# Optimization experiments

Hardware: AMD Instinct MI355X
Metric: run time of the kernel (lower is better)

The kernel has to match this reference:

```python
import jax, jax.numpy as jnp
import numpy as np

M = 5
N = 3
NUM_EPOC = 500
LR = 0.01


def setup_inputs() -> dict:
    key = jax.random.key(0)
    k1, k2, k3, k4, k5 = jax.random.split(key, 5)
    x = jax.random.normal(k1, (8, 32, 32, 128), dtype=jnp.float32)
    weight = jax.random.normal(k2, (3, 3, 128, 256), dtype=jnp.float32) * 0.05
    shiftPara = jax.random.normal(k3, (N,), dtype=jnp.float32) * 0.1
    beta = jax.random.normal(k4, (N,), dtype=jnp.float32)
    alphas_init = jax.random.normal(k5, (M,), dtype=jnp.float32)
    return {"x": x, "weight": weight, "shiftPara": shiftPara, "beta": beta, "alphas_init": alphas_init}


def _binary_weights(w):
    # w: (kh, kw, Cin, Cout). sign(W - mean + shift_i * std), shift_i in linspace(-1, 1, M)
    mean = jnp.mean(w)
    var = jnp.var(w)
    shifts = (-1.0 + jnp.arange(M, dtype=jnp.float32) * (2.0 / (M - 1))) * jnp.sqrt(var)  # (M,)
    return jnp.sign((w - mean)[None] + shifts.reshape(M, 1, 1, 1, 1))  # (M, kh, kw, Cin, Cout)


def _alphas(w, bw, alphas_init):
    # 500-step OLS gradient descent, faithful to the original loop
    flat_w = w.reshape(-1)            # (K,)
    flat_b = bw.reshape(M, -1)        # (M, K)
    K = flat_w.shape[0]

    def step(a, _):
        resid = flat_b.T @ a - flat_w            # (K,)
        grad = (flat_b @ resid) / K              # (M,)
        return a - LR * grad, None

    a, _ = jax.lax.scan(step, alphas_init, None, length=NUM_EPOC)
    return a


def reference(x, weight, shiftPara, beta, alphas_init):
    B, H, W, Cin = x.shape
    kh, kw, _, Cout = weight.shape

    bw = _binary_weights(weight)                       # (M, kh, kw, Cin, Cout)
    alphas = _alphas(weight, bw, alphas_init)          # (M,)

    # N binarized input branches: sign(clip(x + shift_n, 0, 1) - 0.5)
    shifted = jnp.clip(x[None] + shiftPara.reshape(N, 1, 1, 1, 1), 0.0, 1.0)
    bx = jnp.sign(shifted - 0.5)                       # (N, B, H, W, Cin)

    # Fold the M binary bases into output channels -> single conv over N*B images
    w_all = jnp.transpose(bw, (1, 2, 3, 0, 4)).reshape(kh, kw, Cin, M * Cout)
    y = jax.lax.conv_general_dilated(
        bx.reshape(N * B, H, W, Cin), w_all,
        window_strides=(1, 1), padding="SAME",
        dimension_numbers=("NHWC", "HWIO", "NHWC"))     # (N*B, H, W, M*Cout)
    y = y.reshape(N, B, H, W, M, Cout)

    # sum_m alpha_m * conv, then sum_n beta_n * branch
    return jnp.einsum("nbhwmc,m,n->bhwc", y, alphas, beta)
```

## Files before the change

### kernel.cpp

```cpp
#include <hip/hip_runtime.h>
#include <math.h>

#define KW_ELEMS 294912
#define KW_F4    73728
#define LR_GD 0.01
#define NBLK_RED 64
#define NBLK_XE  192
#define NBLK_GC  256

typedef __attribute__((ext_vector_type(8))) short short8;
typedef __attribute__((ext_vector_type(4))) float f32x4;

#define WS_SP_OFF    0
#define WS_GP_OFF    1024
#define WS_WP_OFF    17408
#define WS_XE_OFF    607232
#define XE_CHUNKS    (8 * 34 * 34 * 16)

__device__ __forceinline__ unsigned short f2bf(float f) {
    union { float f; unsigned int u; } v; v.f = f;
    unsigned int r = v.u + 0x7fffu + ((v.u >> 16) & 1u);
    return (unsigned short)(r >> 16);
}

__device__ __forceinline__ void read_stats(const double* sp, double& sw, double& sw2) {
    int lane = threadIdx.x & 63;
    double a = sp[2 * lane];
    double b = sp[2 * lane + 1];
    #pragma unroll
    for (int off = 32; off > 0; off >>= 1) {
        a += __shfl_xor(a, off, 64);
        b += __shfl_xor(b, off, 64);
    }
    sw = a; sw2 = b;
}

__device__ __forceinline__ float xeff_one(float xv, float s0, float s1, float s2,
                                          float be0, float be1, float be2) {
    float v0 = xv + s0, v1 = xv + s1, v2 = xv + s2;
    float g0 = (v0 > 0.5f) ? 1.0f : ((v0 < 0.5f) ? -1.0f : 0.0f);
    float g1 = (v1 > 0.5f) ? 1.0f : ((v1 < 0.5f) ? -1.0f : 0.0f);
    float g2 = (v2 > 0.5f) ? 1.0f : ((v2 < 0.5f) ? -1.0f : 0.0f);
    return be0 * g0 + be1 * g1 + be2 * g2;
}

__global__ __launch_bounds__(256) void k_pre(const float* __restrict__ w,
                                             const float* __restrict__ x,
                                             const float* __restrict__ shiftp,
                                             const float* __restrict__ beta,
                                             void* __restrict__ wsv) {
    int tid = threadIdx.x;

    if (blockIdx.x < NBLK_RED) {
        double* sp = (double*)((char*)wsv + WS_SP_OFF);
        __shared__ double s1[256];
        __shared__ double s2[256];

        double a = 0.0, b = 0.0;
        for (int i4 = blockIdx.x * 256 + tid; i4 < KW_F4; i4 += NBLK_RED * 256) {
            float4 v = *(const float4*)(&w[i4 * 4]);
            a += (double)v.x + (double)v.y + (double)v.z + (double)v.w;
            b += (double)v.x * (double)v.x + (double)v.y * (double)v.y
               + (double)v.z * (double)v.z + (double)v.w * (double)v.w;
        }
        s1[tid] = a; s2[tid] = b;
        __syncthreads();
        for (int off = 128; off > 0; off >>= 1) {
            if (tid < off) { s1[tid] += s1[tid + off]; s2[tid] += s2[tid + off]; }
            __syncthreads();
        }
        if (tid == 0) { sp[blockIdx.x * 2] = s1[0]; sp[blockIdx.x * 2 + 1] = s2[0]; }
    } else {
        unsigned short* xe = (unsigned short*)((char*)wsv + WS_XE_OFF);
        float s0 = shiftp[0], s1v = shiftp[1], s2v = shiftp[2];
        float be0 = beta[0], be1 = beta[1], be2 = beta[2];

        for (int idx = (blockIdx.x - NBLK_RED) * 256 + tid; idx < XE_CHUNKS;
             idx += NBLK_XE * 256) {
            int cb  = idx & 15;
            int c2  = idx >> 4;
            int pos = c2 % 34;
            int t   = c2 / 34;
            int row = t % 34;
            int b   = t / 34;
            int g   = row - 1;
            int wp  = pos - 1;
            unsigned short v[8] = {0, 0, 0, 0, 0, 0, 0, 0};
            if (g >= 0 && g < 32 && wp >= 0 && wp < 32) {
                const float* xp = &x[(((b * 32 + g) * 32) + wp) * 128 + cb * 8];
                float4 x0 = *(const float4*)(xp);
                float4 x1 = *(const float4*)(xp + 4);
                float e[8] = {x0.x, x0.y, x0.z, x0.w, x1.x, x1.y, x1.z, x1.w};
                #pragma unroll
                for (int j = 0; j < 8; j++)
                    v[j] = f2bf(xeff_one(e[j], s0, s1v, s2v, be0, be1, be2));
            }
            int dst = c2 * 256 + ((cb * 16) ^ ((pos & 7) << 4));
            *(short8*)((char*)xe + dst) = *(short8*)v;
        }
    }
}

__global__ __launch_bounds__(256) void k_gc(const float* __restrict__ w,
                                            void* __restrict__ wsv) {
    const double* sp = (const double*)((const char*)wsv + WS_SP_OFF);
    char* gp = (char*)wsv + WS_GP_OFF;

    __shared__ int    lg[4][5];
    __shared__ double lc[4][5];

    int tid  = threadIdx.x;
    int lane = tid & 63;
    int wave = tid >> 6;

    double sw, sw2;
    read_stats(sp, sw, sw2);
    double mean = sw / (double)KW_ELEMS;
    double var  = sw2 / (double)KW_ELEMS - mean * mean;
    float meanf = (float)mean;
    float sigf  = sqrtf((float)var);

    float thr[5];
    #pragma unroll
    for (int m = 0; m < 5; m++) thr[m] = (1.0f - 0.5f * (float)m) * sigf;

    int   cnt[5] = {0, 0, 0, 0, 0};
    float ss[5]  = {0.f, 0.f, 0.f, 0.f, 0.f};
    for (int i4 = blockIdx.x * 256 + tid; i4 < KW_F4; i4 += NBLK_GC * 256) {
        float4 v = *(const float4*)(&w[i4 * 4]);
        float e[4] = {v.x, v.y, v.z, v.w};
        #pragma unroll
        for (int j = 0; j < 4; j++) {
            float base = e[j] - meanf;
            #pragma unroll
            for (int m = 0; m < 5; m++) {
                bool bel = base < thr[m];
                cnt[m] += bel ? 1 : 0;
                ss[m]  += bel ? e[j] : 0.f;
            }
        }
    }
    double sd[5];
    #pragma unroll
    for (int m = 0; m < 5; m++) sd[m] = (double)ss[m];
    #pragma unroll
    for (int m = 0; m < 5; m++) {
        int c = cnt[m]; double s = sd[m];
        #pragma unroll
        for (int off = 32; off > 0; off >>= 1) {
            c += __shfl_xor(c, off, 64);
            s += __shfl_xor(s, off, 64);
        }
        cnt[m] = c; sd[m] = s;
    }
    if (lane == 0) {
        #pragma unroll
        for (int m = 0; m < 5; m++) { lg[wave][m] = cnt[m]; lc[wave][m] = sd[m]; }
    }
    __syncthreads();
    if (tid == 0) {
        int*    pn = (int*)(gp + blockIdx.x * 64);
        double* pS = (double*)(gp + blockIdx.x * 64 + 24);
        #pragma unroll
        for (int m = 0; m < 5; m++) {
            pn[m] = lg[0][m] + lg[1][m] + lg[2][m] + lg[3][m];
            pS[m] = lc[0][m] + lc[1][m] + lc[2][m] + lc[3][m];
        }
    }
}

__global__ __launch_bounds__(256) void k_weff(const float* __restrict__ w,
                                              const float* __restrict__ a0f,
                                              void* __restrict__ wsv) {
    const double* sp = (const double*)((const char*)wsv + WS_SP_OFF);
    const char*   gp = (const char*)wsv + WS_GP_OFF;
    unsigned short* wpk = (unsigned short*)((char*)wsv + WS_WP_OFF);

    __shared__ double Gd[25];
    __shared__ double RmL[25];
    __shared__ double astar_s[5];
    __shared__ float  alph[5];
    __shared__ float  tile[32][64];

    int tid   = threadIdx.x;
    int lane  = tid & 63;
    int tap   = blockIdx.x >> 4;
    int rest  = blockIdx.x & 15;
    int c32   = rest >> 2;
    int cin0  = c32 * 32;
    int cout0 = (rest & 3) * 64;

    int i0 = tid, i1 = tid + 256;
    int ci0 = i0 >> 4, f40 = i0 & 15;
    int ci1 = i1 >> 4, f41 = i1 & 15;
    float4 v0 = *(const float4*)(&w[(tap * 128 + cin0 + ci0) * 256 + cout0 + f40 * 4]);
    float4 v1 = *(const float4*)(&w[(tap * 128 + cin0 + ci1) * 256 + cout0 + f41 * 4]);

    double sw, sw2;
    read_stats(sp, sw, sw2);
    double mean = sw / (double)KW_ELEMS;
    double var  = sw2 / (double)KW_ELEMS - mean * mean;
    float meanf = (float)mean;
    float sigf  = sqrtf((float)var);

    int nred[5]; double Sred[5];
    #pragma unroll
    for (int m = 0; m < 5; m++) { nred[m] = 0; Sred[m] = 0.0; }
    #pragma unroll
    for (int q = 0; q < 4; q++) {
        const int*    pn = (const int*)(gp + (lane + q * 64) * 64);
        const double* pS = (const double*)(gp + (lane + q * 64) * 64 + 24);
        #pragma unroll
        for (int m = 0; m < 5; m++) { nred[m] += pn[m]; Sred[m] += pS[m]; }
    }
    #pragma unroll
    for (int m = 0; m < 5; m++) {
        int c = nred[m]; double s = Sred[m];
        #pragma unroll
        for (int off = 32; off > 0; off >>= 1) {
            c += __shfl_xor(c, off, 64);
            s += __shfl_xor(s, off, 64);
        }
        nred[m] = c; Sred[m] = s;
    }
    double Creg[5];
    #pragma unroll
    for (int m = 0; m < 5; m++)
        Creg[m] = (sw - 2.0 * Sred[m]) / (double)KW_ELEMS;

    double Rg = 0.0, Ag = 0.0;
    {
        int i = tid / 5, j = tid % 5;
        if (tid < 25) {
            double v;
            if (i == j) v = 1.0;
            else {
                int d = nred[i] - nred[j];
                if (d < 0) d = -d;
                v = ((double)KW_ELEMS - 2.0 * (double)d) / (double)KW_ELEMS;
            }
            Gd[tid] = v;
            Ag = ((i == j) ? 1.0 : 0.0) - LR_GD * v;
            Rg = Ag;
        }
    }
    __syncthreads();

    if (tid == 64) {
        double L[25];
        #pragma unroll
        for (int i = 0; i < 25; i++) L[i] = 0.0;
        #pragma unroll
        for (int i = 0; i < 5; i++) {
            #pragma unroll
            for (int j = 0; j <= i; j++) {
                double s = Gd[i * 5 + j];
                #pragma unroll
                for (int k = 0; k < j; k++) s -= L[i * 5 + k] * L[j * 5 + k];
                if (i == j) L[i * 5 + j] = sqrt(s);
                else        L[i * 5 + j] = s / L[j * 5 + j];
            }
        }
        double y[5], astar[5];
        #pragma unroll
        for (int i = 0; i < 5; i++) {
            double s = Creg[i];
            #pragma unroll
            for (int k = 0; k < i; k++) s -= L[i * 5 + k] * y[k];
            y[i] = s / L[i * 5 + i];
        }
        #pragma unroll
        for (int ii2 = 0; ii2 < 5; ii2++) {
            int i = 4 - ii2;
            double s = y[i];
            #pragma unroll
            for (int k = 0; k < 5; k++) if (k > i) s -= L[k * 5 + i] * astar[k];
            astar[i] = s / L[i * 5 + i];
        }
        #pragma unroll
        for (int i = 0; i < 5; i++) astar_s[i] = astar[i];
    }

    if (tid < 25) {
        int i = tid / 5, j = tid % 5;
        const int bits[8] = {1, 1, 1, 1, 0, 1, 0, 0};
        #pragma unroll
        for (int s = 0; s < 8; s++) {
            double t = 0.0;
            #pragma unroll
            for (int k = 0; k < 5; k++) {
                double rik = __shfl(Rg, i * 5 + k, 64);
                double rkj = __shfl(Rg, k * 5 + j, 64);
                t += rik * rkj;
            }
            if (bits[s]) {
                double r2 = 0.0;
                #pragma unroll
                for (int k = 0; k < 5; k++) {
                    double tik = __shfl(t, i * 5 + k, 64);
                    double akj = __shfl(Ag, k * 5 + j, 64);
                    r2 += tik * akj;
                }
                Rg = r2;
            } else {
                Rg = t;
            }
        }
        RmL[tid] = Rg;
    }
    __syncthreads();

    if (tid < 5) {
        double s = astar_s[tid];
        #pragma unroll
        for (int j = 0; j < 5; j++)
            s += RmL[tid * 5 + j] * ((double)a0f[j] - astar_s[j]);
        alph[tid] = (float)s;
    }
    __syncthreads();

    float al[5] = {alph[0], alph[1], alph[2], alph[3], alph[4]};

    {
        float r[4] = {v0.x, v0.y, v0.z, v0.w};
        #pragma unroll
        for (int j = 0; j < 4; j++) {
            float base = r[j] - meanf;
            float acc = 0.0f;
            #pragma unroll
            for (int m = 0; m < 5; m++) {
                float arg = base + (-1.0f + 0.5f * (float)m) * sigf;
                float s = (arg > 0.0f) ? 1.0f : ((arg < 0.0f) ? -1.0f : 0.0f);
                acc += al[m] * s;
            }
            tile[ci0][f40 * 4 + j] = acc;
        }
        float r1[4] = {v1.x, v1.y, v1.z, v1.w};
        #pragma unroll
        for (int j = 0; j < 4; j++) {
            float base = r1[j] - meanf;
            float acc = 0.0f;
            #pragma unroll
            for (int m = 0; m < 5; m++) {
                float arg = base + (-1.0f + 0.5f * (float)m) * sigf;
                float s = (arg > 0.0f) ? 1.0f : ((arg < 0.0f) ? -1.0f : 0.0f);
                acc += al[m] * s;
            }
            tile[ci1][f41 * 4 + j] = acc;
        }
    }
    __syncthreads();

    int cc  = tid & 63;
    int kg  = tid >> 6;
    unsigned short ob[8];
    #pragma unroll
    for (int k = 0; k < 8; k++) ob[k] = f2bf(tile[kg * 8 + k][cc]);
    unsigned short* dst = wpk + (((tap * 16 + c32 * 4 + kg) * 256) + cout0 + cc) * 8;
    *(short8*)dst = *(short8*)ob;
}

__global__ __launch_bounds__(256, 2) void k_conv(
    const void* __restrict__ wsv, float* __restrict__ out) {
    const unsigned short* wp = (const unsigned short*)((const char*)wsv + WS_WP_OFF);
    const char* xe = (const char*)wsv + WS_XE_OFF;
    __shared__ __align__(16) unsigned short ldsx[3 * 34 * 128];

    int bid = blockIdx.x;
    int ch  = bid & 1;
    int h   = (bid >> 1) & 31;
    int b   = bid >> 6;
    int tid = threadIdx.x;

    const char* src = xe + ((b * 34 + h) * 34) * 256;
    #pragma unroll 2
    for (int i = tid; i < 1632; i += 256) {
        *(short8*)((char*)ldsx + i * 16) = *(const short8*)(src + i * 16);
    }
    __syncthreads();

    int lane = tid & 63;
    int wave = tid >> 6;
    int l15  = lane & 15;
    int kg   = lane >> 4;
    int coutbase = (ch << 7) + wave * 32;

    f32x4 acc[2][2];
    #pragma unroll
    for (int mt = 0; mt < 2; mt++)
        #pragma unroll
        for (int nt = 0; nt < 2; nt++) acc[mt][nt] = (f32x4){0.f, 0.f, 0.f, 0.f};

    const unsigned short* wbase = wp + ((kg * 256) + coutbase + l15) * 8;

    short8 bc[8], bn[8];
    #pragma unroll
    for (int q = 0; q < 4; q++) {
        bc[2 * q]     = *(const short8*)(wbase + q * 8192);
        bc[2 * q + 1] = *(const short8*)(wbase + q * 8192 + 128);
    }

    #pragma unroll
    for (int dh = 0; dh < 3; dh++) {
        #pragma unroll
        for (int dw = 0; dw < 3; dw++) {
            int tap = dh * 3 + dw;
            if (tap < 8) {
                const unsigned short* wnx = wbase + (tap + 1) * 32768;
                #pragma unroll
                for (int q = 0; q < 4; q++) {
                    bn[2 * q]     = *(const short8*)(wnx + q * 8192);
                    bn[2 * q + 1] = *(const short8*)(wnx + q * 8192 + 128);
                }
            }
            int r0  = dh * 34 + l15 + dw;
            int r1  = r0 + 16;
            int key = ((l15 + dw) & 7) << 4;
            #pragma unroll
            for (int q = 0; q < 4; q++) {
                int cbyte = q * 64 + kg * 16;
                short8 a0f8 = *(const short8*)((const char*)ldsx +
                               (r0 * 256 + (cbyte ^ key)));
                short8 a1f8 = *(const short8*)((const char*)ldsx +
                               (r1 * 256 + (cbyte ^ key)));
                acc[0][0] = __builtin_amdgcn_mfma_f32_16x16x32_bf16(a0f8, bc[2*q],   acc[0][0], 0, 0, 0);
                acc[0][1] = __builtin_amdgcn_mfma_f32_16x16x32_bf16(a0f8, bc[2*q+1], acc[0][1], 0, 0, 0);
                acc[1][0] = __builtin_amdgcn_mfma_f32_16x16x32_bf16(a1f8, bc[2*q],   acc[1][0], 0, 0, 0);
                acc[1][1] = __builtin_amdgcn_mfma_f32_16x16x32_bf16(a1f8, bc[2*q+1], acc[1][1], 0, 0, 0);
            }
            if (tap < 8) {
                #pragma unroll
                for (int i = 0; i < 8; i++) bc[i] = bn[i];
            }
        }
    }

    #pragma unroll
    for (int mt = 0; mt < 2; mt++) {
        #pragma unroll
        for (int nt = 0; nt < 2; nt++) {
            int col = coutbase + nt * 16 + l15;
            #pragma unroll
            for (int reg = 0; reg < 4; reg++) {
                int row = mt * 16 + kg * 4 + reg;
                out[(((b * 32 + h) * 32) + row) * 256 + col] = acc[mt][nt][reg];
            }
        }
    }
}

extern "C" void kernel_launch(void* const* d_in, const int* in_sizes, int n_in,
                              void* d_out, int out_size, void* d_ws, size_t ws_size,
                              hipStream_t stream) {
    const float* x      = (const float*)d_in[0];
    const float* w      = (const float*)d_in[1];
    const float* shiftp = (const float*)d_in[2];
    const float* beta   = (const float*)d_in[3];
    const float* a0     = (const float*)d_in[4];
    float* out = (float*)d_out;

    k_pre<<<NBLK_RED + NBLK_XE, 256, 0, stream>>>(w, x, shiftp, beta, d_ws);
    k_gc<<<NBLK_GC, 256, 0, stream>>>(w, d_ws);
    k_weff<<<144, 256, 0, stream>>>(w, a0, d_ws);
    k_conv<<<512, 256, 0, stream>>>(d_ws, out);
}
```

Measured before the change: 30.49 us.

## Split input binarization across k_gc and k_weff to fill idle blocks

The input-encoding work (xe) moves out of the first preprocessing kernel and is split into two halves. Each half runs on extra blocks appended to k_gc and to k_weff, so it overlaps the latency-bound weight-statistics and alpha/weight-packing stages. k_pre now only does the weight sum reduction with 64 blocks. The intent is to shorten the critical path by using idle CUs in the small kernels. The risk is that the extra blocks compete with the stages they share a kernel with and lengthen them.

New measurement: 31.36 us. 1.03x slower.

```diff
diff --git a/kernel.cpp b/kernel.cpp
--- a/kernel.cpp
+++ b/kernel.cpp
@@ -5,8 +5,8 @@
 #define KW_F4    73728
 #define LR_GD 0.01
 #define NBLK_RED 64
-#define NBLK_XE  192
 #define NBLK_GC  256
+#define NBLK_XR  128
 
 typedef __attribute__((ext_vector_type(8))) short short8;
 typedef __attribute__((ext_vector_type(4))) float f32x4;
@@ -16,6 +16,7 @@
 #define WS_WP_OFF    17408
 #define WS_XE_OFF    607232
 #define XE_CHUNKS    (8 * 34 * 34 * 16)
+#define XE_HALF      (XE_CHUNKS / 2)
 
 __device__ __forceinline__ unsigned short f2bf(float f) {
     union { float f; unsigned int u; } v; v.f = f;
@@ -44,65 +45,74 @@
     return be0 * g0 + be1 * g1 + be2 * g2;
 }
 
+__device__ __forceinline__ void xe_produce(const float* __restrict__ x,
+                                           const float* __restrict__ shiftp,
+                                           const float* __restrict__ beta,
+                                           char* __restrict__ wsv,
+                                           int blk, int nblk, int c0, int c1) {
+    unsigned short* xe = (unsigned short*)(wsv + WS_XE_OFF);
+    float s0 = shiftp[0], s1v = shiftp[1], s2v = shiftp[2];
+    float be0 = beta[0], be1 = beta[1], be2 = beta[2];
+    int tid = threadIdx.x;
+
+    for (int idx = c0 + blk * 256 + tid; idx < c1; idx += nblk * 256) {
+        int cb  = idx & 15;
+        int c2  = idx >> 4;
+        int pos = c2 % 34;
+        int t   = c2 / 34;
+        int row = t % 34;
+        int b   = t / 34;
+        int g   = row - 1;
+        int wp  = pos - 1;
+        unsigned short v[8] = {0, 0, 0, 0, 0, 0, 0, 0};
+        if (g >= 0 && g < 32 && wp >= 0 && wp < 32) {
+            const float* xp = &x[(((b * 32 + g) * 32) + wp) * 128 + cb * 8];
+            float4 x0 = *(const float4*)(xp);
+            float4 x1 = *(const float4*)(xp + 4);
+            float e[8] = {x0.x, x0.y, x0.z, x0.w, x1.x, x1.y, x1.z, x1.w};
+            #pragma unroll
+            for (int j = 0; j < 8; j++)
+                v[j] = f2bf(xeff_one(e[j], s0, s1v, s2v, be0, be1, be2));
+        }
+        int dst = c2 * 256 + ((cb * 16) ^ ((pos & 7) << 4));
+        *(short8*)((char*)xe + dst) = *(short8*)v;
+    }
+}
+
 __global__ __launch_bounds__(256) void k_pre(const float* __restrict__ w,
-                                             const float* __restrict__ x,
-                                             const float* __restrict__ shiftp,
-                                             const float* __restrict__ beta,
                                              void* __restrict__ wsv) {
     int tid = threadIdx.x;
-
-    if (blockIdx.x < NBLK_RED) {
-        double* sp = (double*)((char*)wsv + WS_SP_OFF);
-        __shared__ double s1[256];
-        __shared__ double s2[256];
-
-        double a = 0.0, b = 0.0;
-        for (int i4 = blockIdx.x * 256 + tid; i4 < KW_F4; i4 += NBLK_RED * 256) {
-            float4 v = *(const float4*)(&w[i4 * 4]);
-            a += (double)v.x + (double)v.y + (double)v.z + (double)v.w;
-            b += (double)v.x * (double)v.x + (double)v.y * (double)v.y
-               + (double)v.z * (double)v.z + (double)v.w * (double)v.w;
-        }
-        s1[tid] = a; s2[tid] = b;
+    double* sp = (double*)((char*)wsv + WS_SP_OFF);
+    __shared__ double s1[256];
+    __shared__ double s2[256];
+
+    double a = 0.0, b = 0.0;
+    for (int i4 = blockIdx.x * 256 + tid; i4 < KW_F4; i4 += NBLK_RED * 256) {
+        float4 v = *(const float4*)(&w[i4 * 4]);
+        a += (double)v.x + (double)v.y + (double)v.z + (double)v.w;
+        b += (double)v.x * (double)v.x + (double)v.y * (double)v.y
+           + (double)v.z * (double)v.z + (double)v.w * (double)v.w;
+    }
+    s1[tid] = a; s2[tid] = b;
+    __syncthreads();
+    for (int off = 128; off > 0; off >>= 1) {
+        if (tid < off) { s1[tid] += s1[tid + off]; s2[tid] += s2[tid + off]; }
         __syncthreads();
-        for (int off = 128; off > 0; off >>= 1) {
-            if (tid < off) { s1[tid] += s1[tid + off]; s2[tid] += s2[tid + off]; }
-            __syncthreads();
-        }
-        if (tid == 0) { sp[blockIdx.x * 2] = s1[0]; sp[blockIdx.x * 2 + 1] = s2[0]; }
-    } else {
-        unsigned short* xe = (unsigned short*)((char*)wsv + WS_XE_OFF);
-        float s0 = shiftp[0], s1v = shiftp[1], s2v = shiftp[2];
-        float be0 = beta[0], be1 = beta[1], be2 = beta[2];
-
-        for (int idx = (blockIdx.x - NBLK_RED) * 256 + tid; idx < XE_CHUNKS;
-             idx += NBLK_XE * 256) {
-            int cb  = idx & 15;
-            int c2  = idx >> 4;
-            int pos = c2 % 34;
-            int t   = c2 / 34;
-            int row = t % 34;
-            int b   = t / 34;
-            int g   = row - 1;
-            int wp  = pos - 1;
-            unsigned short v[8] = {0, 0, 0, 0, 0, 0, 0, 0};
-            if (g >= 0 && g < 32 && wp >= 0 && wp < 32) {
-                const float* xp = &x[(((b * 32 + g) * 32) + wp) * 128 + cb * 8];
-                float4 x0 = *(const float4*)(xp);
-                float4 x1 = *(const float4*)(xp + 4);
-                float e[8] = {x0.x, x0.y, x0.z, x0.w, x1.x, x1.y, x1.z, x1.w};
-                #pragma unroll
-                for (int j = 0; j < 8; j++)
-                    v[j] = f2bf(xeff_one(e[j], s0, s1v, s2v, be0, be1, be2));
-            }
-            int dst = c2 * 256 + ((cb * 16) ^ ((pos & 7) << 4));
-            *(short8*)((char*)xe + dst) = *(short8*)v;
-        }
-    }
+    }
+    if (tid == 0) { sp[blockIdx.x * 2] = s1[0]; sp[blockIdx.x * 2 + 1] = s2[0]; }
 }
 
 __global__ __launch_bounds__(256) void k_gc(const float* __restrict__ w,
+                                            const float* __restrict__ x,
+                                            const float* __restrict__ shiftp,
+                                            const float* __restrict__ beta,
                                             void* __restrict__ wsv) {
+    if (blockIdx.x >= NBLK_GC) {
+        xe_produce(x, shiftp, beta, (char*)wsv,
+                   blockIdx.x - NBLK_GC, NBLK_XR, 0, XE_HALF);
+        return;
+    }
+
     const double* sp = (const double*)((const char*)wsv + WS_SP_OFF);
     char* gp = (char*)wsv + WS_GP_OFF;
 
@@ -171,7 +181,16 @@
 
 __global__ __launch_bounds__(256) void k_weff(const float* __restrict__ w,
                                               const float* __restrict__ a0f,
+                                              const float* __restrict__ x,
+                                              const float* __restrict__ shiftp,
+                                              const float* __restrict__ beta,
                                               void* __restrict__ wsv) {
+    if (blockIdx.x >= 144) {
+        xe_produce(x, shiftp, beta, (char*)wsv,
+                   blockIdx.x - 144, NBLK_XR, XE_HALF, XE_CHUNKS);
+        return;
+    }
+
     const double* sp = (const double*)((const char*)wsv + WS_SP_OFF);
     const char*   gp = (const char*)wsv + WS_GP_OFF;
     unsigned short* wpk = (unsigned short*)((char*)wsv + WS_WP_OFF);
@@ -459,8 +478,8 @@
     const float* a0     = (const float*)d_in[4];
     float* out = (float*)d_out;
 
-    k_pre<<<NBLK_RED + NBLK_XE, 256, 0, stream>>>(w, x, shiftp, beta, d_ws);
-    k_gc<<<NBLK_GC, 256, 0, stream>>>(w, d_ws);
-    k_weff<<<144, 256, 0, stream>>>(w, a0, d_ws);
+    k_pre<<<NBLK_RED, 256, 0, stream>>>(w, d_ws);
+    k_gc<<<NBLK_GC + NBLK_XR, 256, 0, stream>>>(w, x, shiftp, beta, d_ws);
+    k_weff<<<144 + NBLK_XR, 256, 0, stream>>>(w, a0, x, shiftp, beta, d_ws);
     k_conv<<<512, 256, 0, stream>>>(d_ws, out);
 }
```
